# Optimization experiments

Hardware: AMD Instinct MI355X
Metric: run time of the kernel (lower is better)

Reference implementation:

```python
import jax, jax.numpy as jnp
import numpy as np
import math

N_HEADS = 32
N_KV_HEADS = 8
MAX_SEQ_LEN = 2048


def _rope_cos_sin(seq_len, head_dim, dtype):
    # precompute_freqs_cis: theta=10000, positions 0..seq_len-1 (note: NOT offset by start_pos, faithful to source)
    inv_freq = 1.0 / (10000.0 ** (jnp.arange(0, head_dim, 2, dtype=jnp.float32) / head_dim))
    t = jnp.arange(seq_len, dtype=jnp.float32)
    angles = jnp.outer(t, inv_freq)  # [S, hd/2]
    return jnp.cos(angles).astype(dtype), jnp.sin(angles).astype(dtype)


def _apply_rope(x, cos, sin):
    # x: [B, S, H, hd]; rotate consecutive pairs (llama complex convention)
    B, S, H, hd = x.shape
    xr = x.reshape(B, S, H, hd // 2, 2)
    x1, x2 = xr[..., 0], xr[..., 1]
    c = cos[None, :, None, :]
    s = sin[None, :, None, :]
    o1 = x1 * c - x2 * s
    o2 = x1 * s + x2 * c
    return jnp.stack([o1, o2], axis=-1).reshape(B, S, H, hd)


def setup_inputs() -> dict:
    key = jax.random.key(0)
    ks = jax.random.split(key, 5)
    dim = 4096
    B, S = 1, 2048
    sd = 1.0 / math.sqrt(dim)
    return {
        "x": jax.random.normal(ks[0], (B, S, dim), dtype=jnp.float32),
        "wq": jax.random.normal(ks[1], (4096, 4096), dtype=jnp.float32) * sd,
        "wk": jax.random.normal(ks[2], (1024, 4096), dtype=jnp.float32) * sd,
        "wv": jax.random.normal(ks[3], (1024, 4096), dtype=jnp.float32) * sd,
        "wo": jax.random.normal(ks[4], (4096, 4096), dtype=jnp.float32) * sd,
        "start_pos": 0,
    }


def reference(x, wq, wk, wv, wo, start_pos):
    B, S, D = x.shape
    Hq, Hkv = N_HEADS, N_KV_HEADS
    hd = D // Hq
    n_rep = Hq // Hkv

    xq = (x @ wq.T).reshape(B, S, Hq, hd)
    xk = (x @ wk.T).reshape(B, S, Hkv, hd)
    xv = (x @ wv.T).reshape(B, S, Hkv, hd)

    cos, sin = _rope_cos_sin(S, hd, x.dtype)
    xq = _apply_rope(xq, cos, sin)
    xk = _apply_rope(xk, cos, sin)

    # KV cache append + read back [:, :start_pos+S] (start_pos is a static Python int)
    cache_k = jnp.zeros((B, MAX_SEQ_LEN, Hkv, hd), dtype=x.dtype)
    cache_v = jnp.zeros((B, MAX_SEQ_LEN, Hkv, hd), dtype=x.dtype)
    cache_k = jax.lax.dynamic_update_slice(cache_k, xk, (0, start_pos, 0, 0))
    cache_v = jax.lax.dynamic_update_slice(cache_v, xv, (0, start_pos, 0, 0))
    kv_len = start_pos + S
    keys = cache_k[:, :kv_len]    # [B, K, Hkv, hd]
    values = cache_v[:, :kv_len]

    # GQA repeat_kv: [B, K, Hkv, hd] -> [B, K, Hq, hd]
    keys = jnp.broadcast_to(keys[:, :, :, None, :], (B, kv_len, Hkv, n_rep, hd)).reshape(B, kv_len, Hq, hd)
    values = jnp.broadcast_to(values[:, :, :, None, :], (B, kv_len, Hkv, n_rep, hd)).reshape(B, kv_len, Hq, hd)

    scale = 1.0 / math.sqrt(hd)
    scores = jnp.einsum('bqhd,bkhd->bhqk', xq, keys) * scale  # [B, Hq, S, K]
    # NOTE: source applies NO causal mask — faithful reproduction
    attn = jax.nn.softmax(scores, axis=-1)
    out = jnp.einsum('bhqk,bkhd->bqhd', attn, values).reshape(B, S, Hq * hd)
    return out @ wo.T
```

## Files before the change

kernel.cpp:

```cpp
#include <hip/hip_runtime.h>
#include <hip/hip_bf16.h>

typedef _Float16 f16_t;
typedef unsigned int uint;
typedef __attribute__((ext_vector_type(8))) _Float16 f16x8;
typedef __attribute__((ext_vector_type(4))) _Float16 f16x4;
typedef __attribute__((ext_vector_type(4))) float f32x4;
typedef __attribute__((ext_vector_type(16))) float f32x16;

#define ROPE_C (13.287712379549449f / 64.0f)

__global__ __launch_bounds__(256) void repack_x16(const float* __restrict__ src,
                                                  uint16_t* __restrict__ dh)
{
    const int p  = blockIdx.y;
    const int kb = blockIdx.x;
    const int tid = threadIdx.x;
    const int rr = tid >> 3;
    const int k4 = tid & 7;
    const int slot = k4 >> 1;
    const int so   = (k4 & 1) * 4;
    uint16_t* bh = dh + ((size_t)p * 128 + kb) * 4096;
    #pragma unroll
    for (int it = 0; it < 4; ++it) {
        const int r = it * 32 + rr;
        const float4 v = *reinterpret_cast<const float4*>(
            &src[((size_t)p * 128 + r) * 4096 + kb * 32 + k4 * 4]);
        float f[4] = {v.x, v.y, v.z, v.w};
        f16x4 h;
        #pragma unroll
        for (int e = 0; e < 4; ++e) h[e] = (f16_t)f[e];
        const int pos = r * 32 + ((slot ^ ((r >> 1) & 3)) << 3) + so;
        *reinterpret_cast<f16x4*>(&bh[pos]) = h;
    }
}

__global__ __launch_bounds__(256) void repack_w96_16(const float* __restrict__ wq,
                                                     const float* __restrict__ wk,
                                                     const float* __restrict__ wv,
                                                     uint16_t* __restrict__ dst)
{
    const int kb  = blockIdx.x;
    const int pan = blockIdx.y;
    const int tid = threadIdx.x;
    const int k4 = tid & 7;
    const int slot = k4 >> 1;
    const int so   = (k4 & 1) * 4;
    uint16_t* bh = dst + ((size_t)pan * 128 + kb) * 3072;
    #pragma unroll
    for (int it = 0; it < 3; ++it) {
        const int r = it * 32 + (tid >> 3);
        const int n = pan * 96 + r;
        const float* srow = (n < 4096) ? (wq + (size_t)n * 4096)
                          : (n < 5120) ? (wk + (size_t)(n - 4096) * 4096)
                                       : (wv + (size_t)(n - 5120) * 4096);
        const float4 v = *reinterpret_cast<const float4*>(srow + kb * 32 + k4 * 4);
        float f[4] = {v.x, v.y, v.z, v.w};
        f16x4 h;
        #pragma unroll
        for (int e = 0; e < 4; ++e) h[e] = (f16_t)f[e];
        const int pos = r * 32 + ((slot ^ ((r >> 1) & 3)) << 3) + so;
        *reinterpret_cast<f16x4*>(&bh[pos]) = h;
    }
}

__global__ __launch_bounds__(256) void repack_h16(const float* __restrict__ src,
                                                  uint16_t* __restrict__ dh)
{
    const int p  = blockIdx.y;
    const int kb = blockIdx.x;
    const int tid = threadIdx.x;
    const int rr = tid >> 3;
    const int k4 = tid & 7;
    const int slot = k4 >> 1;
    const int so   = (k4 & 1) * 4;
    uint16_t* bh = dh + ((size_t)p * 128 + kb) * 4096;
    #pragma unroll
    for (int it = 0; it < 4; ++it) {
        const int r = it * 32 + rr;
        const float4 v = *reinterpret_cast<const float4*>(
            &src[((size_t)p * 128 + r) * 4096 + kb * 32 + k4 * 4]);
        float f[4] = {v.x, v.y, v.z, v.w};
        f16x4 h;
        #pragma unroll
        for (int e = 0; e < 4; ++e) h[e] = (f16_t)f[e];
        const int pos = r * 32 + ((slot ^ ((r >> 1) & 3)) << 3) + so;
        *reinterpret_cast<f16x4*>(&bh[pos]) = h;
    }
}

__global__ __launch_bounds__(512) void gemm_qkv9(const uint16_t* __restrict__ xh,
                                                 const uint16_t* __restrict__ wqkv,
                                                 uint16_t* __restrict__ xq16,
                                                 uint16_t* __restrict__ xk16,
                                                 uint16_t* __restrict__ xv16)
{
    __shared__ char lds[2][40960];

    const int bid = blockIdx.x;
    const int xcd = bid & 7;
    const int i_  = bid >> 3;
    const int by = (xcd & 1) * 8 + (i_ & 7);
    const int bx = (xcd >> 1) * 8 + (i_ >> 3);
    const int tid = threadIdx.x;
    const int w = tid >> 6, lane = tid & 63;
    const int wm = w >> 2, wn = w & 3;
    const int fr = lane & 15, s4 = lane >> 4;

    const uint16_t* sp[5];
    int dof[5];
    int stridec[5];
    #pragma unroll
    for (int i = 0; i < 5; ++i) {
        const int c = w + 8 * i;
        if (c < 16) {
            const int kk = c >> 3, inner = c & 7;
            sp[i] = xh + (size_t)by * 524288 + kk * 4096 + inner * 512 + lane * 8;
            dof[i] = c * 1024;
            stridec[i] = 8192;
        } else {
            const int cb = c - 16;
            const int pan = cb / 12, rem = cb % 12;
            const int kk = rem / 6, inner = rem % 6;
            sp[i] = wqkv + (size_t)(bx * 2 + pan) * 393216 + kk * 3072 + inner * 512 + lane * 8;
            dof[i] = 16384 + cb * 1024;
            stridec[i] = 6144;
        }
    }

    f32x4 acc[4][3] = {};

    #pragma unroll
    for (int i = 0; i < 5; ++i)
        __builtin_amdgcn_global_load_lds(
            (const __attribute__((address_space(1))) void*)(sp[i]),
            (__attribute__((address_space(3))) void*)(&lds[0][0] + dof[i]), 16, 0, 0);
    asm volatile("s_waitcnt vmcnt(0)" ::: "memory");
    __builtin_amdgcn_s_barrier();
    __builtin_amdgcn_sched_barrier(0);

    for (int t = 0; t < 64; ++t) {
        const char* b = &lds[t & 1][0];
        if (t + 1 < 64) {
            char* nb = &lds[(t + 1) & 1][0];
            #pragma unroll
            for (int i = 0; i < 5; ++i)
                __builtin_amdgcn_global_load_lds(
                    (const __attribute__((address_space(1))) void*)(sp[i] + (size_t)(t + 1) * stridec[i]),
                    (__attribute__((address_space(3))) void*)(nb + dof[i]), 16, 0, 0);
        }
        #pragma unroll
        for (int kk = 0; kk < 2; ++kk) {
            f16x8 fb[3];
            #pragma unroll
            for (int j = 0; j < 3; ++j) {
                const int cbp = wn * 48 + j * 16 + fr;
                const int pan = (cbp >= 96) ? 1 : 0;
                const int rb = cbp - pan * 96;
                fb[j] = *reinterpret_cast<const f16x8*>(
                    b + 16384 + pan * 12288 + kk * 6144 + rb * 64 + ((s4 ^ ((rb >> 1) & 3)) << 4));
            }
            #pragma unroll
            for (int ri = 0; ri < 4; ++ri) {
                const int rloc = wm * 64 + ri * 16 + fr;
                f16x8 fh = *reinterpret_cast<const f16x8*>(
                    b + kk * 8192 + rloc * 64 + ((s4 ^ ((rloc >> 1) & 3)) << 4));
                __builtin_amdgcn_s_setprio(1);
                #pragma unroll
                for (int j = 0; j < 3; ++j)
                    acc[ri][j] = __builtin_amdgcn_mfma_f32_16x16x32_f16(fh, fb[j], acc[ri][j], 0, 0, 0);
                __builtin_amdgcn_s_setprio(0);
            }
        }
        asm volatile("s_waitcnt vmcnt(0)" ::: "memory");
        __builtin_amdgcn_s_barrier();
        __builtin_amdgcn_sched_barrier(0);
    }

    const int r0 = by * 128 + wm * 64 + s4 * 4;
    const int c0 = bx * 192 + wn * 48 + fr;
    #pragma unroll
    for (int ri = 0; ri < 4; ++ri)
        #pragma unroll
        for (int j = 0; j < 3; ++j) {
            const int col = c0 + j * 16;
            #pragma unroll
            for (int rr = 0; rr < 4; ++rr) {
                const int row = r0 + ri * 16 + rr;
                const f16_t v = (f16_t)acc[ri][j][rr];
                uint16_t bits;
                __builtin_memcpy(&bits, &v, 2);
                if (col < 4096)      xq16[(size_t)row * 4096 + col] = bits;
                else if (col < 5120) xk16[(size_t)row * 1024 + (col - 4096)] = bits;
                else                 xv16[(size_t)row * 1024 + (col - 5120)] = bits;
            }
        }
}

__global__ __launch_bounds__(512) void gemm_out8(const uint16_t* __restrict__ aoh,
                                                 const uint16_t* __restrict__ woh,
                                                 float* __restrict__ out)
{
    __shared__ char lds[2][49152];

    const int bid = blockIdx.x;
    const int xcd = bid & 7;
    const int i_  = bid >> 3;
    const int by = (xcd & 1) * 4 + (i_ & 3);
    const int bx = (xcd >> 1) * 8 + (i_ >> 2);
    const int tid = threadIdx.x;
    const int w = tid >> 6, lane = tid & 63;
    const int wm = w >> 2, wn = w & 3;
    const int fr = lane & 15, s4 = lane >> 4;

    const uint16_t* sp[6];
    int dof[6];
    #pragma unroll
    for (int i = 0; i < 6; ++i) {
        const int c = w + 8 * i;
        if (c < 32) {
            const int pan = c >> 4, sub = c & 15;
            sp[i] = aoh + (size_t)(2 * by + pan) * 524288 + sub * 512 + lane * 8;
            dof[i] = c * 1024;
        } else {
            sp[i] = woh + (size_t)bx * 524288 + (c - 32) * 512 + lane * 8;
            dof[i] = 32768 + (c - 32) * 1024;
        }
    }

    f32x4 acc[8][2] = {};

    #pragma unroll
    for (int i = 0; i < 6; ++i)
        __builtin_amdgcn_global_load_lds(
            (const __attribute__((address_space(1))) void*)(sp[i]),
            (__attribute__((address_space(3))) void*)(&lds[0][0] + dof[i]), 16, 0, 0);
    asm volatile("s_waitcnt vmcnt(0)" ::: "memory");
    __builtin_amdgcn_s_barrier();
    __builtin_amdgcn_sched_barrier(0);

    for (int t = 0; t < 64; ++t) {
        const char* b = &lds[t & 1][0];
        if (t + 1 < 64) {
            char* nb = &lds[(t + 1) & 1][0];
            #pragma unroll
            for (int i = 0; i < 6; ++i)
                __builtin_amdgcn_global_load_lds(
                    (const __attribute__((address_space(1))) void*)(sp[i] + (size_t)(t + 1) * 8192),
                    (__attribute__((address_space(3))) void*)(nb + dof[i]), 16, 0, 0);
        }
        #pragma unroll
        for (int kk = 0; kk < 2; ++kk) {
            f16x8 fb[2];
            #pragma unroll
            for (int j = 0; j < 2; ++j) {
                const int cbp = wn * 32 + j * 16 + fr;
                fb[j] = *reinterpret_cast<const f16x8*>(
                    b + 32768 + kk * 8192 + cbp * 64 + ((s4 ^ ((cbp >> 1) & 3)) << 4));
            }
            #pragma unroll
            for (int p = 0; p < 4; ++p) {
                f16x8 fh[2];
                #pragma unroll
                for (int f = 0; f < 2; ++f) {
                    const int rloc = p * 32 + f * 16 + fr;
                    fh[f] = *reinterpret_cast<const f16x8*>(
                        b + wm * 16384 + kk * 8192 + rloc * 64 + ((s4 ^ ((rloc >> 1) & 3)) << 4));
                }
                __builtin_amdgcn_s_setprio(1);
                #pragma unroll
                for (int f = 0; f < 2; ++f)
                    #pragma unroll
                    for (int j = 0; j < 2; ++j)
                        acc[p * 2 + f][j] = __builtin_amdgcn_mfma_f32_16x16x32_f16(fh[f], fb[j], acc[p * 2 + f][j], 0, 0, 0);
                __builtin_amdgcn_s_setprio(0);
            }
        }
        asm volatile("s_waitcnt vmcnt(0)" ::: "memory");
        __builtin_amdgcn_s_barrier();
        __builtin_amdgcn_sched_barrier(0);
    }

    const int r0 = by * 256 + wm * 128 + s4 * 4;
    const int c0 = bx * 128 + wn * 32 + fr;
    #pragma unroll
    for (int ri = 0; ri < 8; ++ri)
        #pragma unroll
        for (int j = 0; j < 2; ++j)
            #pragma unroll
            for (int rr = 0; rr < 4; ++rr)
                out[(size_t)(r0 + ri * 16 + rr) * 4096 + c0 + j * 16] = acc[ri][j][rr];
}

__global__ __launch_bounds__(256) void conv_kv(const uint16_t* __restrict__ xk16,
                                               const uint16_t* __restrict__ xv16,
                                               uint16_t* __restrict__ kvg)
{
    __shared__ float V[32][129];
    const int t = blockIdx.x;
    const int h = blockIdx.y;
    const int tid = threadIdx.x;
    uint16_t* tile = kvg + ((size_t)(h * 64 + t)) * 8192;

    #pragma unroll
    for (int i = 0; i < 4; ++i) {
        const int v = i * 256 + tid;
        const int row = v >> 5, c4 = (v & 31) * 4;
        f16x4 hv = *reinterpret_cast<const f16x4*>(&xv16[(size_t)(t * 32 + row) * 1024 + h * 128 + c4]);
        #pragma unroll
        for (int e = 0; e < 4; ++e) V[row][c4 + e] = (float)hv[e];
    }

    {
        const int r = tid >> 3;
        const int d0 = (tid & 7) * 16;
        const int pos_ = t * 32 + r;
        float f[16];
        const uint16_t* kr = &xk16[(size_t)pos_ * 1024 + h * 128 + d0];
        f16x8 k0 = *reinterpret_cast<const f16x8*>(kr);
        f16x8 k1 = *reinterpret_cast<const f16x8*>(kr + 8);
        #pragma unroll
        for (int e = 0; e < 8; ++e) { f[e] = (float)k0[e]; f[8 + e] = (float)k1[e]; }
        #pragma unroll
        for (int i = 0; i < 8; ++i) {
            const int j = (d0 >> 1) + i;
            const float invf = exp2f(-(float)j * ROPE_C);
            const float ang = (float)pos_ * invf;
            float sn, cs;
            __sincosf(ang, &sn, &cs);
            const float x1 = f[2 * i], x2 = f[2 * i + 1];
            f[2 * i]     = x1 * cs - x2 * sn;
            f[2 * i + 1] = x1 * sn + x2 * cs;
        }
        #pragma unroll
        for (int cc = 0; cc < 2; ++cc) {
            f16x8 hv;
            #pragma unroll
            for (int e = 0; e < 8; ++e) hv[e] = (f16_t)f[cc * 8 + e];
            const int c = (d0 >> 3) + cc;
            const int pos = r * 128 + ((c ^ (r & 15)) << 3);
            *reinterpret_cast<f16x8*>(&tile[pos]) = hv;
        }
    }
    __syncthreads();
    {
        const int d = tid >> 1;
        const int k0 = (tid & 1) * 16;
        float g[16];
        #pragma unroll
        for (int j = 0; j < 16; ++j) g[j] = V[k0 + j][d];
        #pragma unroll
        for (int cc = 0; cc < 2; ++cc) {
            f16x8 hv;
            #pragma unroll
            for (int e = 0; e < 8; ++e) hv[e] = (f16_t)g[cc * 8 + e];
            const int c = (k0 >> 3) + cc;
            const int pos = 4096 + d * 32 + ((c ^ ((d >> 1) & 3)) << 3);
            *reinterpret_cast<f16x8*>(&tile[pos]) = hv;
        }
    }
}

__device__ __forceinline__ uint cvtpkh(float lo, float hi) {
    uint r;
    asm("v_cvt_pkrtz_f16_f32 %0, %1, %2" : "=v"(r) : "v"(lo), "v"(hi));
    return r;
}
__device__ __forceinline__ void permswap(uint& a, uint& b) {
    asm("v_permlane32_swap_b32 %0, %1" : "+v"(a), "+v"(b));
}
__device__ __forceinline__ f16x8 pack4h(uint w0, uint w1, uint w2, uint w3) {
    union { uint u[4]; f16x8 v; } t;
    t.u[0] = w0; t.u[1] = w1; t.u[2] = w2; t.u[3] = w3;
    return t.v;
}

__global__ __launch_bounds__(512, 2) void attn_mfma(const uint16_t* __restrict__ xq16,
                                                    const uint16_t* __restrict__ kvg,
                                                    uint16_t* __restrict__ aoh)
{
    __shared__ char lds[2][16384];

    const int b = blockIdx.x;
    const int kvh = b & 7;
    const int r = b >> 3;
    const int h = kvh * 4 + (r & 3);
    const int q0 = (r >> 2) * 256;
    const int tid = threadIdx.x;
    const int w = tid >> 6;
    const int lane = tid & 63;
    const int ln31 = lane & 31;
    const int hi = lane >> 5;

    const int q = q0 + w * 32 + ln31;
    const uint16_t* qrow = xq16 + (size_t)q * 4096 + h * 128;
    f16x8 Qh[8];
    #pragma unroll
    for (int ks = 0; ks < 8; ++ks) {
        const int dbase = ks * 16 + hi * 8;
        f16x8 raw = *reinterpret_cast<const f16x8*>(qrow + dbase);
        float f[8];
        #pragma unroll
        for (int e = 0; e < 8; ++e) f[e] = (float)raw[e];
        #pragma unroll
        for (int i = 0; i < 4; ++i) {
            const int j = (dbase >> 1) + i;
            const float invf = exp2f(-(float)j * ROPE_C);
            const float ang = (float)q * invf;
            float sn, cs;
            __sincosf(ang, &sn, &cs);
            const float x1 = f[2 * i], x2 = f[2 * i + 1];
            f[2 * i]     = (x1 * cs - x2 * sn) * 0.08838834764831845f;
            f[2 * i + 1] = (x1 * sn + x2 * cs) * 0.08838834764831845f;
        }
        #pragma unroll
        for (int e = 0; e < 8; ++e) Qh[ks][e] = (f16_t)f[e];
    }

    const char* gkv = (const char*)kvg + (size_t)kvh * 64 * 16384;

    f32x16 oacc[4] = {{}, {}, {}, {}};
    float m = -3.0e38f, l = 0.f;

    {
        #pragma unroll
        for (int i = 0; i < 2; ++i) {
            const int chunk = i * 8 + w;
            __builtin_amdgcn_global_load_lds(
                (const __attribute__((address_space(1))) void*)(gkv + chunk * 1024 + lane * 16),
                (__attribute__((address_space(3))) void*)(&lds[0][chunk * 1024]),
                16, 0, 0);
        }
    }

    for (int t = 0; t < 64; ++t) {
        __syncthreads();
        if (t + 1 < 64) {
            const char* g = gkv + (size_t)(t + 1) * 16384;
            const int buf = (t + 1) & 1;
            #pragma unroll
            for (int i = 0; i < 2; ++i) {
                const int chunk = i * 8 + w;
                __builtin_amdgcn_global_load_lds(
                    (const __attribute__((address_space(1))) void*)(g + chunk * 1024 + lane * 16),
                    (__attribute__((address_space(3))) void*)(&lds[buf][chunk * 1024]),
                    16, 0, 0);
            }
        }
        const int cur = t & 1;
        const char* Kf = lds[cur];
        const char* Vf = lds[cur] + 8192;

        f32x16 s0 = {}, s1 = {};
        __builtin_amdgcn_s_setprio(1);
        #pragma unroll
        for (int ks = 0; ks < 8; ++ks) {
            const int byt = ln31 * 256 + ((ks * 32 + hi * 16) ^ ((ln31 & 15) << 4));
            f16x8 a = *reinterpret_cast<const f16x8*>(Kf + byt);
            if (ks & 1) s1 = __builtin_amdgcn_mfma_f32_32x32x16_f16(a, Qh[ks], s1, 0, 0, 0);
            else        s0 = __builtin_amdgcn_mfma_f32_32x32x16_f16(a, Qh[ks], s0, 0, 0, 0);
        }
        __builtin_amdgcn_s_setprio(0);
        f32x16 s = s0 + s1;

        float pmax = s[0];
        #pragma unroll
        for (int jj = 1; jj < 16; ++jj) pmax = fmaxf(pmax, s[jj]);
        pmax = fmaxf(pmax, __shfl_xor(pmax, 32));
        if (!__all(pmax - m <= 8.0f)) {
            const float mnew = fmaxf(m, pmax);
            const float corr = __expf(m - mnew);
            l *= corr;
            #pragma unroll
            for (int dt = 0; dt < 4; ++dt) oacc[dt] *= corr;
            m = mnew;
        }
        float psum = 0.f;
        #pragma unroll
        for (int jj = 0; jj < 16; ++jj) {
            float pv = __expf(s[jj] - m);
            s[jj] = pv;
            psum += pv;
        }
        psum += __shfl_xor(psum, 32);
        l += psum;

        #pragma unroll
        for (int ks = 0; ks < 2; ++ks) {
            const int b0 = ks * 8;
            uint wa = cvtpkh(s[b0 + 0], s[b0 + 1]);
            uint wb = cvtpkh(s[b0 + 2], s[b0 + 3]);
            uint wc = cvtpkh(s[b0 + 4], s[b0 + 5]);
            uint wd = cvtpkh(s[b0 + 6], s[b0 + 7]);
            permswap(wa, wc); permswap(wb, wd);
            f16x8 Pf = pack4h(wa, wb, wc, wd);
            __builtin_amdgcn_s_setprio(1);
            #pragma unroll
            for (int dt = 0; dt < 4; ++dt) {
                const int row = dt * 32 + ln31;
                const int byt = row * 64 + ((ks * 32 + hi * 16) ^ (((row >> 1) & 3) << 4));
                f16x8 vh = *reinterpret_cast<const f16x8*>(Vf + byt);
                oacc[dt] = __builtin_amdgcn_mfma_f32_32x32x16_f16(vh, Pf, oacc[dt], 0, 0, 0);
            }
            __builtin_amdgcn_s_setprio(0);
        }
    }

    const float invl = 1.0f / l;
    const int p   = q >> 7;
    const int rr_ = q & 127;
    const int rsw = (rr_ >> 1) & 3;
    #pragma unroll
    for (int dt = 0; dt < 4; ++dt) {
        const int kb = h * 4 + dt;
        uint16_t* bh = aoh + ((size_t)p * 128 + kb) * 4096;
        #pragma unroll
        for (int g4 = 0; g4 < 4; ++g4) {
            f16x4 hv;
            #pragma unroll
            for (int e = 0; e < 4; ++e)
                hv[e] = (f16_t)(oacc[dt][g4 * 4 + e] * invl);
            const int pos = rr_ * 32 + ((g4 ^ rsw) << 3) + 4 * hi;
            *reinterpret_cast<f16x4*>(&bh[pos]) = hv;
        }
    }
}

extern "C" void kernel_launch(void* const* d_in, const int* in_sizes, int n_in,
                              void* d_out, int out_size, void* d_ws, size_t ws_size,
                              hipStream_t stream)
{
    const float* x  = (const float*)d_in[0];
    const float* wq = (const float*)d_in[1];
    const float* wk = (const float*)d_in[2];
    const float* wv = (const float*)d_in[3];
    const float* wo = (const float*)d_in[4];
    float* out = (float*)d_out;

    float* ws = (float*)d_ws;
    uint16_t* xq16 = (uint16_t*)ws;
    uint16_t* kvg  = (uint16_t*)(ws + 8388608);
    uint16_t* xk16 = (uint16_t*)(ws + 12582912);
    uint16_t* xv16 = (uint16_t*)(ws + 14680064);
    uint16_t* aoh  = (uint16_t*)(ws + 12582912);
    uint16_t* xh   = (uint16_t*)(ws + 20971520);
    uint16_t* wqkv = (uint16_t*)(ws + 29360128);
    uint16_t* woh  = (uint16_t*)(ws + 41943040);

    dim3 blk(256);
    repack_x16   <<<dim3(128, 16), blk, 0, stream>>>(x, xh);
    repack_w96_16<<<dim3(128, 64), blk, 0, stream>>>(wq, wk, wv, wqkv);
    gemm_qkv9    <<<dim3(512), dim3(512), 0, stream>>>(xh, wqkv, xq16, xk16, xv16);
    repack_h16   <<<dim3(128, 32), blk, 0, stream>>>(wo, woh);
    conv_kv      <<<dim3(64, 8), blk, 0, stream>>>(xk16, xv16, kvg);
    attn_mfma    <<<dim3(256), dim3(512), 0, stream>>>(xq16, kvg, aoh);
    gemm_out8    <<<dim3(256), dim3(512), 0, stream>>>(aoh, woh, out);
}
```

Baseline: 347.0 us.

## Fuse fp32-to-fp16 weight conversion into QKV and output GEMM tile loads

Removes the separate weight repack kernels and has both GEMMs load fp32 weights straight from global memory into registers, convert them to fp16, and write them into the swizzled LDS layout inside the double-buffered loop. This saves writing and re-reading the fp16 weight copies in HBM and drops two launches. In exchange, each weight tile is fetched and converted several times, once per block row that uses it, at twice the byte size. Register-staged loads also replace the async global-to-LDS path for the B operand, which may hurt overlap between loads and MFMA work.

```diff
diff --git a/kernel.cpp b/kernel.cpp
--- a/kernel.cpp
+++ b/kernel.cpp
@@ -35,65 +35,13 @@
     }
 }
 
-__global__ __launch_bounds__(256) void repack_w96_16(const float* __restrict__ wq,
-                                                     const float* __restrict__ wk,
-                                                     const float* __restrict__ wv,
-                                                     uint16_t* __restrict__ dst)
-{
-    const int kb  = blockIdx.x;
-    const int pan = blockIdx.y;
-    const int tid = threadIdx.x;
-    const int k4 = tid & 7;
-    const int slot = k4 >> 1;
-    const int so   = (k4 & 1) * 4;
-    uint16_t* bh = dst + ((size_t)pan * 128 + kb) * 3072;
-    #pragma unroll
-    for (int it = 0; it < 3; ++it) {
-        const int r = it * 32 + (tid >> 3);
-        const int n = pan * 96 + r;
-        const float* srow = (n < 4096) ? (wq + (size_t)n * 4096)
-                          : (n < 5120) ? (wk + (size_t)(n - 4096) * 4096)
-                                       : (wv + (size_t)(n - 5120) * 4096);
-        const float4 v = *reinterpret_cast<const float4*>(srow + kb * 32 + k4 * 4);
-        float f[4] = {v.x, v.y, v.z, v.w};
-        f16x4 h;
-        #pragma unroll
-        for (int e = 0; e < 4; ++e) h[e] = (f16_t)f[e];
-        const int pos = r * 32 + ((slot ^ ((r >> 1) & 3)) << 3) + so;
-        *reinterpret_cast<f16x4*>(&bh[pos]) = h;
-    }
-}
-
-__global__ __launch_bounds__(256) void repack_h16(const float* __restrict__ src,
-                                                  uint16_t* __restrict__ dh)
-{
-    const int p  = blockIdx.y;
-    const int kb = blockIdx.x;
-    const int tid = threadIdx.x;
-    const int rr = tid >> 3;
-    const int k4 = tid & 7;
-    const int slot = k4 >> 1;
-    const int so   = (k4 & 1) * 4;
-    uint16_t* bh = dh + ((size_t)p * 128 + kb) * 4096;
-    #pragma unroll
-    for (int it = 0; it < 4; ++it) {
-        const int r = it * 32 + rr;
-        const float4 v = *reinterpret_cast<const float4*>(
-            &src[((size_t)p * 128 + r) * 4096 + kb * 32 + k4 * 4]);
-        float f[4] = {v.x, v.y, v.z, v.w};
-        f16x4 h;
-        #pragma unroll
-        for (int e = 0; e < 4; ++e) h[e] = (f16_t)f[e];
-        const int pos = r * 32 + ((slot ^ ((r >> 1) & 3)) << 3) + so;
-        *reinterpret_cast<f16x4*>(&bh[pos]) = h;
-    }
-}
-
-__global__ __launch_bounds__(512) void gemm_qkv9(const uint16_t* __restrict__ xh,
-                                                 const uint16_t* __restrict__ wqkv,
-                                                 uint16_t* __restrict__ xq16,
-                                                 uint16_t* __restrict__ xk16,
-                                                 uint16_t* __restrict__ xv16)
+__global__ __launch_bounds__(512) void gemm_qkv10(const uint16_t* __restrict__ xh,
+                                                  const float* __restrict__ wq,
+                                                  const float* __restrict__ wk,
+                                                  const float* __restrict__ wv,
+                                                  uint16_t* __restrict__ xq16,
+                                                  uint16_t* __restrict__ xk16,
+                                                  uint16_t* __restrict__ xv16)
 {
     __shared__ char lds[2][40960];
 
@@ -107,47 +55,74 @@
     const int wm = w >> 2, wn = w & 3;
     const int fr = lane & 15, s4 = lane >> 4;
 
-    const uint16_t* sp[5];
-    int dof[5];
-    int stridec[5];
-    #pragma unroll
-    for (int i = 0; i < 5; ++i) {
+    const uint16_t* spA[2];
+    int dofA[2];
+    #pragma unroll
+    for (int i = 0; i < 2; ++i) {
         const int c = w + 8 * i;
-        if (c < 16) {
-            const int kk = c >> 3, inner = c & 7;
-            sp[i] = xh + (size_t)by * 524288 + kk * 4096 + inner * 512 + lane * 8;
-            dof[i] = c * 1024;
-            stridec[i] = 8192;
-        } else {
-            const int cb = c - 16;
-            const int pan = cb / 12, rem = cb % 12;
-            const int kk = rem / 6, inner = rem % 6;
-            sp[i] = wqkv + (size_t)(bx * 2 + pan) * 393216 + kk * 3072 + inner * 512 + lane * 8;
-            dof[i] = 16384 + cb * 1024;
-            stridec[i] = 6144;
-        }
+        spA[i] = xh + (size_t)by * 524288 + (c >> 3) * 4096 + (c & 7) * 512 + lane * 8;
+        dofA[i] = c * 1024;
+    }
+
+    const float* bsrc[3];
+    int boff[3];
+    #pragma unroll
+    for (int i = 0; i < 3; ++i) {
+        const int v = tid + 512 * i;
+        const int row = v >> 3;
+        const int s8  = v & 7;
+        const int n = bx * 192 + row;
+        const float* srow = (n < 4096) ? (wq + (size_t)n * 4096)
+                          : (n < 5120) ? (wk + (size_t)(n - 4096) * 4096)
+                                       : (wv + (size_t)(n - 5120) * 4096);
+        bsrc[i] = srow + s8 * 8;
+        const int pan = (row >= 96) ? 1 : 0;
+        const int rb = row - pan * 96;
+        boff[i] = 16384 + pan * 12288 + (s8 >> 2) * 6144 + rb * 64 + (((s8 & 3) ^ ((rb >> 1) & 3)) << 4);
     }
 
     f32x4 acc[4][3] = {};
-
-    #pragma unroll
-    for (int i = 0; i < 5; ++i)
+    float4 br[3][2];
+
+    #pragma unroll
+    for (int i = 0; i < 2; ++i)
         __builtin_amdgcn_global_load_lds(
-            (const __attribute__((address_space(1))) void*)(sp[i]),
-            (__attribute__((address_space(3))) void*)(&lds[0][0] + dof[i]), 16, 0, 0);
+            (const __attribute__((address_space(1))) void*)(spA[i]),
+            (__attribute__((address_space(3))) void*)(&lds[0][0] + dofA[i]), 16, 0, 0);
+    #pragma unroll
+    for (int i = 0; i < 3; ++i) {
+        br[i][0] = *reinterpret_cast<const float4*>(bsrc[i]);
+        br[i][1] = *reinterpret_cast<const float4*>(bsrc[i] + 4);
+    }
     asm volatile("s_waitcnt vmcnt(0)" ::: "memory");
+    #pragma unroll
+    for (int i = 0; i < 3; ++i) {
+        f16x8 hx;
+        hx[0] = (f16_t)br[i][0].x; hx[1] = (f16_t)br[i][0].y;
+        hx[2] = (f16_t)br[i][0].z; hx[3] = (f16_t)br[i][0].w;
+        hx[4] = (f16_t)br[i][1].x; hx[5] = (f16_t)br[i][1].y;
+        hx[6] = (f16_t)br[i][1].z; hx[7] = (f16_t)br[i][1].w;
+        *reinterpret_cast<f16x8*>(&lds[0][0] + boff[i]) = hx;
+    }
+    asm volatile("s_waitcnt lgkmcnt(0)" ::: "memory");
     __builtin_amdgcn_s_barrier();
     __builtin_amdgcn_sched_barrier(0);
 
     for (int t = 0; t < 64; ++t) {
         const char* b = &lds[t & 1][0];
-        if (t + 1 < 64) {
-            char* nb = &lds[(t + 1) & 1][0];
-            #pragma unroll
-            for (int i = 0; i < 5; ++i)
+        char* nb = &lds[(t + 1) & 1][0];
+        const bool pre = (t + 1 < 64);
+        if (pre) {
+            #pragma unroll
+            for (int i = 0; i < 3; ++i) {
+                br[i][0] = *reinterpret_cast<const float4*>(bsrc[i] + (size_t)(t + 1) * 64);
+                br[i][1] = *reinterpret_cast<const float4*>(bsrc[i] + (size_t)(t + 1) * 64 + 4);
+            }
+            #pragma unroll
+            for (int i = 0; i < 2; ++i)
                 __builtin_amdgcn_global_load_lds(
-                    (const __attribute__((address_space(1))) void*)(sp[i] + (size_t)(t + 1) * stridec[i]),
-                    (__attribute__((address_space(3))) void*)(nb + dof[i]), 16, 0, 0);
+                    (const __attribute__((address_space(1))) void*)(spA[i] + (size_t)(t + 1) * 8192),
+                    (__attribute__((address_space(3))) void*)(nb + dofA[i]), 16, 0, 0);
         }
         #pragma unroll
         for (int kk = 0; kk < 2; ++kk) {
@@ -173,6 +148,18 @@
             }
         }
         asm volatile("s_waitcnt vmcnt(0)" ::: "memory");
+        if (pre) {
+            #pragma unroll
+            for (int i = 0; i < 3; ++i) {
+                f16x8 hx;
+                hx[0] = (f16_t)br[i][0].x; hx[1] = (f16_t)br[i][0].y;
+                hx[2] = (f16_t)br[i][0].z; hx[3] = (f16_t)br[i][0].w;
+                hx[4] = (f16_t)br[i][1].x; hx[5] = (f16_t)br[i][1].y;
+                hx[6] = (f16_t)br[i][1].z; hx[7] = (f16_t)br[i][1].w;
+                *reinterpret_cast<f16x8*>(nb + boff[i]) = hx;
+            }
+        }
+        asm volatile("s_waitcnt lgkmcnt(0)" ::: "memory");
         __builtin_amdgcn_s_barrier();
         __builtin_amdgcn_sched_barrier(0);
     }
@@ -197,9 +184,9 @@
         }
 }
 
-__global__ __launch_bounds__(512) void gemm_out8(const uint16_t* __restrict__ aoh,
-                                                 const uint16_t* __restrict__ woh,
-                                                 float* __restrict__ out)
+__global__ __launch_bounds__(512) void gemm_out10(const uint16_t* __restrict__ aoh,
+                                                  const float* __restrict__ wo,
+                                                  float* __restrict__ out)
 {
     __shared__ char lds[2][49152];
 
@@ -213,41 +200,68 @@
     const int wm = w >> 2, wn = w & 3;
     const int fr = lane & 15, s4 = lane >> 4;
 
-    const uint16_t* sp[6];
-    int dof[6];
-    #pragma unroll
-    for (int i = 0; i < 6; ++i) {
+    const uint16_t* spA[4];
+    int dofA[4];
+    #pragma unroll
+    for (int i = 0; i < 4; ++i) {
         const int c = w + 8 * i;
-        if (c < 32) {
-            const int pan = c >> 4, sub = c & 15;
-            sp[i] = aoh + (size_t)(2 * by + pan) * 524288 + sub * 512 + lane * 8;
-            dof[i] = c * 1024;
-        } else {
-            sp[i] = woh + (size_t)bx * 524288 + (c - 32) * 512 + lane * 8;
-            dof[i] = 32768 + (c - 32) * 1024;
-        }
+        spA[i] = aoh + (size_t)(2 * by + (c >> 4)) * 524288 + (c & 15) * 512 + lane * 8;
+        dofA[i] = c * 1024;
+    }
+
+    const float* bsrc[2];
+    int boff[2];
+    #pragma unroll
+    for (int i = 0; i < 2; ++i) {
+        const int v = tid + 512 * i;
+        const int row = v >> 3;
+        const int s8  = v & 7;
+        bsrc[i] = wo + (size_t)(bx * 128 + row) * 4096 + s8 * 8;
+        boff[i] = 32768 + (s8 >> 2) * 8192 + row * 64 + (((s8 & 3) ^ ((row >> 1) & 3)) << 4);
     }
 
     f32x4 acc[8][2] = {};
-
-    #pragma unroll
-    for (int i = 0; i < 6; ++i)
+    float4 br[2][2];
+
+    #pragma unroll
+    for (int i = 0; i < 4; ++i)
         __builtin_amdgcn_global_load_lds(
-            (const __attribute__((address_space(1))) void*)(sp[i]),
-            (__attribute__((address_space(3))) void*)(&lds[0][0] + dof[i]), 16, 0, 0);
+            (const __attribute__((address_space(1))) void*)(spA[i]),
+            (__attribute__((address_space(3))) void*)(&lds[0][0] + dofA[i]), 16, 0, 0);
+    #pragma unroll
+    for (int i = 0; i < 2; ++i) {
+        br[i][0] = *reinterpret_cast<const float4*>(bsrc[i]);
+        br[i][1] = *reinterpret_cast<const float4*>(bsrc[i] + 4);
+    }
     asm volatile("s_waitcnt vmcnt(0)" ::: "memory");
+    #pragma unroll
+    for (int i = 0; i < 2; ++i) {
+        f16x8 hx;
+        hx[0] = (f16_t)br[i][0].x; hx[1] = (f16_t)br[i][0].y;
+        hx[2] = (f16_t)br[i][0].z; hx[3] = (f16_t)br[i][0].w;
+        hx[4] = (f16_t)br[i][1].x; hx[5] = (f16_t)br[i][1].y;
+        hx[6] = (f16_t)br[i][1].z; hx[7] = (f16_t)br[i][1].w;
+        *reinterpret_cast<f16x8*>(&lds[0][0] + boff[i]) = hx;
+    }
+    asm volatile("s_waitcnt lgkmcnt(0)" ::: "memory");
     __builtin_amdgcn_s_barrier();
     __builtin_amdgcn_sched_barrier(0);
 
     for (int t = 0; t < 64; ++t) {
         const char* b = &lds[t & 1][0];
-        if (t + 1 < 64) {
-            char* nb = &lds[(t + 1) & 1][0];
-            #pragma unroll
-            for (int i = 0; i < 6; ++i)
+        char* nb = &lds[(t + 1) & 1][0];
+        const bool pre = (t + 1 < 64);
+        if (pre) {
+            #pragma unroll
+            for (int i = 0; i < 2; ++i) {
+                br[i][0] = *reinterpret_cast<const float4*>(bsrc[i] + (size_t)(t + 1) * 64);
+                br[i][1] = *reinterpret_cast<const float4*>(bsrc[i] + (size_t)(t + 1) * 64 + 4);
+            }
+            #pragma unroll
+            for (int i = 0; i < 4; ++i)
                 __builtin_amdgcn_global_load_lds(
-                    (const __attribute__((address_space(1))) void*)(sp[i] + (size_t)(t + 1) * 8192),
-                    (__attribute__((address_space(3))) void*)(nb + dof[i]), 16, 0, 0);
+                    (const __attribute__((address_space(1))) void*)(spA[i] + (size_t)(t + 1) * 8192),
+                    (__attribute__((address_space(3))) void*)(nb + dofA[i]), 16, 0, 0);
         }
         #pragma unroll
         for (int kk = 0; kk < 2; ++kk) {
@@ -277,6 +291,18 @@
             }
         }
         asm volatile("s_waitcnt vmcnt(0)" ::: "memory");
+        if (pre) {
+            #pragma unroll
+            for (int i = 0; i < 2; ++i) {
+                f16x8 hx;
+                hx[0] = (f16_t)br[i][0].x; hx[1] = (f16_t)br[i][0].y;
+                hx[2] = (f16_t)br[i][0].z; hx[3] = (f16_t)br[i][0].w;
+                hx[4] = (f16_t)br[i][1].x; hx[5] = (f16_t)br[i][1].y;
+                hx[6] = (f16_t)br[i][1].z; hx[7] = (f16_t)br[i][1].w;
+                *reinterpret_cast<f16x8*>(nb + boff[i]) = hx;
+            }
+        }
+        asm volatile("s_waitcnt lgkmcnt(0)" ::: "memory");
         __builtin_amdgcn_s_barrier();
         __builtin_amdgcn_sched_barrier(0);
     }
@@ -544,15 +570,11 @@
     uint16_t* xv16 = (uint16_t*)(ws + 14680064);
     uint16_t* aoh  = (uint16_t*)(ws + 12582912);
     uint16_t* xh   = (uint16_t*)(ws + 20971520);
-    uint16_t* wqkv = (uint16_t*)(ws + 29360128);
-    uint16_t* woh  = (uint16_t*)(ws + 41943040);
 
     dim3 blk(256);
-    repack_x16   <<<dim3(128, 16), blk, 0, stream>>>(x, xh);
-    repack_w96_16<<<dim3(128, 64), blk, 0, stream>>>(wq, wk, wv, wqkv);
-    gemm_qkv9    <<<dim3(512), dim3(512), 0, stream>>>(xh, wqkv, xq16, xk16, xv16);
-    repack_h16   <<<dim3(128, 32), blk, 0, stream>>>(wo, woh);
-    conv_kv      <<<dim3(64, 8), blk, 0, stream>>>(xk16, xv16, kvg);
-    attn_mfma    <<<dim3(256), dim3(512), 0, stream>>>(xq16, kvg, aoh);
-    gemm_out8    <<<dim3(256), dim3(512), 0, stream>>>(aoh, woh, out);
-}
+    repack_x16<<<dim3(128, 16), blk, 0, stream>>>(x, xh);
+    gemm_qkv10<<<dim3(512), dim3(512), 0, stream>>>(xh, wq, wk, wv, xq16, xk16, xv16);
+    conv_kv   <<<dim3(64, 8), blk, 0, stream>>>(xk16, xv16, kvg);
+    attn_mfma <<<dim3(256), dim3(512), 0, stream>>>(xq16, kvg, aoh);
+    gemm_out10<<<dim3(256), dim3(512), 0, stream>>>(aoh, wo, out);
+}
```

After: 395.8 us. +14.1%, slower.
